# Kernel optimization log

Measured on AMD Instinct MI355X. Metric: run time of the kernel, lower is better.

## Reference

```python
import jax, jax.numpy as jnp
import numpy as np

N_NODES = 50000
N_EDGES = 800000
IN_DIM = 128
HID = 2 * IN_DIM          # GCNConv out channels = input_dims * 2
FC1 = 1024
FC2 = 512
N_ACT = 16
N_AGENTS = 8192
EPS = 1e-5


def setup_inputs() -> dict:
    key = jax.random.key(0)
    ks = jax.random.split(key, 12)
    def gl(k, shape):  # glorot-ish init for weights
        fan = shape[0]
        return jax.random.normal(k, shape, jnp.float32) / jnp.sqrt(jnp.float32(fan))
    return {
        "x": jax.random.normal(ks[0], (N_NODES, IN_DIM), jnp.float32),
        "edge_index": jax.random.randint(ks[1], (2, N_EDGES), 0, N_NODES, jnp.int32),
        "agent_idx": jax.random.randint(ks[2], (N_AGENTS,), 0, N_NODES, jnp.int32),
        "W_gcn": gl(ks[3], (IN_DIM, HID)),
        "b_gcn": jnp.zeros((HID,), jnp.float32),
        "W1": gl(ks[4], (HID, FC1)),
        "b1": jnp.zeros((FC1,), jnp.float32),
        "g1": jnp.ones((FC1,), jnp.float32),
        "be1": jnp.zeros((FC1,), jnp.float32),
        "W2": gl(ks[5], (FC1, FC2)),
        "b2": jnp.zeros((FC2,), jnp.float32),
        "g2": jnp.ones((FC2,), jnp.float32),
        "be2": jnp.zeros((FC2,), jnp.float32),
        "Wmu": gl(ks[6], (FC2, N_ACT)) * 0.003,
        "bmu": jnp.zeros((N_ACT,), jnp.float32),
    }


def _layernorm(h, g, b):
    mu = jnp.mean(h, axis=-1, keepdims=True)
    var = jnp.mean(jnp.square(h - mu), axis=-1, keepdims=True)
    return (h - mu) * jax.lax.rsqrt(var + EPS) * g + b


def _gcn_conv(x, edge_index, W, b):
    # PyG GCNConv: add self-loops, symmetric normalization, linear, scatter-add.
    n = x.shape[0]
    loop = jnp.arange(n, dtype=edge_index.dtype)
    src = jnp.concatenate([edge_index[0], loop])   # [E+N]
    dst = jnp.concatenate([edge_index[1], loop])   # [E+N]
    deg = jax.ops.segment_sum(jnp.ones_like(dst, jnp.float32), dst, num_segments=n)
    dis = jnp.where(deg > 0, jax.lax.rsqrt(jnp.maximum(deg, 1.0)), 0.0)
    norm = dis[src] * dis[dst]                     # [E+N]
    xw = x @ W                                     # [N, HID]
    msg = xw[src] * norm[:, None]                  # gather + scale
    return jax.ops.segment_sum(msg, dst, num_segments=n) + b


def reference(x, edge_index, agent_idx, W_gcn, b_gcn, W1, b1, g1, be1,
              W2, b2, g2, be2, Wmu, bmu):
    h = _gcn_conv(x, edge_index, W_gcn, b_gcn)     # [N, HID]
    h = h[agent_idx]                               # masked selection -> [A, HID]
    h = jax.nn.relu(h)
    h = jax.nn.relu(_layernorm(h @ W1 + b1, g1, be1))
    h = jax.nn.relu(_layernorm(h @ W2 + b2, g2, be2))
    return jax.nn.sigmoid(h @ Wmu + bmu)           # [A, N_ACT]
```

## Files before the change

kernel.cpp:

```cpp
#include <hip/hip_runtime.h>
#include <hip/hip_bf16.h>
#include <math.h>

#define N_NODES  50000
#define N_EDGES  800000
#define IN_DIM   128
#define HID      256
#define FC1      1024
#define FC2      512
#define N_ACT    16
#define N_AGENTS 8192

#define BK       64
#define LDK      72
#define BM       128
#define BN       128

#define EB_STRIDE    64

#define SCAT_CHUNK   2048
#define SCAT_BLOCKS  ((N_EDGES + SCAT_CHUNK - 1) / SCAT_CHUNK)
#define N_BUCKETS    196
#define BUCKET_CAP   4608
#define WTR_BLOCKS   208
#define CLAIM_BLOCKS (N_AGENTS / 256)

typedef short bf16x8 __attribute__((ext_vector_type(8)));
typedef float floatx4 __attribute__((ext_vector_type(4)));

__device__ __forceinline__ unsigned short f2b(float f) {
    union { float f; unsigned int i; } v;
    v.f = f;
    unsigned int lsb = (v.i >> 16) & 1u;
    v.i += 0x7fffu + lsb;
    return (unsigned short)(v.i >> 16);
}

__device__ __forceinline__ float b2f(unsigned short u) {
    union { unsigned int i; float f; } v;
    v.i = ((unsigned int)u) << 16;
    return v.f;
}

__device__ __forceinline__ void wtr_block(int b, int tid,
    const float* __restrict__ Wgcn, const float* __restrict__ W1,
    const float* __restrict__ W2, const float* __restrict__ Wmu,
    unsigned short* __restrict__ wgcn_t, unsigned short* __restrict__ w1_t,
    unsigned short* __restrict__ w2_t, unsigned short* __restrict__ wmu_t,
    unsigned short (*Ts)[72]) {
    const float* src; unsigned short* dstw; int K, N, tk, tn;
    if (b < 8)        { src = Wgcn; dstw = wgcn_t; K = IN_DIM; N = HID;  tk = b >> 2;        tn = b & 3; }
    else if (b < 72)  { int bb = b - 8;  src = W1; dstw = w1_t; K = HID;  N = FC1;  tk = bb >> 4; tn = bb & 15; }
    else if (b < 200) { int bb = b - 72; src = W2; dstw = w2_t; K = FC1;  N = FC2;  tk = bb >> 3; tn = bb & 7; }
    else              { int bb = b - 200; src = Wmu; dstw = wmu_t; K = FC2; N = N_ACT; tk = bb;   tn = 0; }
    int k0 = tk * 64, n0 = tn * 64;
    int r = tid >> 2;
    int cc = (tid & 3) * 16;
    if (n0 + cc < N) {
        const float* p = src + (size_t)(k0 + r) * N + n0 + cc;
        #pragma unroll
        for (int i = 0; i < 16; i += 4) {
            float4 v = *(const float4*)(p + i);
            Ts[r][cc + i + 0] = f2b(v.x);
            Ts[r][cc + i + 1] = f2b(v.y);
            Ts[r][cc + i + 2] = f2b(v.z);
            Ts[r][cc + i + 3] = f2b(v.w);
        }
    }
    __syncthreads();
    int n = tid >> 2;
    if (n0 + n < N) {
        bf16x8 o0, o1;
        #pragma unroll
        for (int i = 0; i < 8; ++i) o0[i] = (short)Ts[cc + i][n];
        #pragma unroll
        for (int i = 0; i < 8; ++i) o1[i] = (short)Ts[cc + 8 + i][n];
        unsigned short* q = dstw + (size_t)(n0 + n) * K + k0 + cc;
        *(bf16x8*)q = o0;
        *(bf16x8*)(q + 8) = o1;
    }
}

__global__ __launch_bounds__(256) void scat_k(const int* __restrict__ src,
                                              const int* __restrict__ dst,
                                              const int* __restrict__ agent_idx,
                                              int* __restrict__ nid,
                                              int* __restrict__ bcnt,
                                              unsigned long long* __restrict__ pairbuf,
                                              const float* __restrict__ Wgcn,
                                              const float* __restrict__ W1,
                                              const float* __restrict__ W2,
                                              const float* __restrict__ Wmu,
                                              unsigned short* __restrict__ wgcn_t,
                                              unsigned short* __restrict__ w1_t,
                                              unsigned short* __restrict__ w2_t,
                                              unsigned short* __restrict__ wmu_t) {
    __shared__ unsigned short Ts[64][72];
    __shared__ int hist[N_BUCKETS], base[N_BUCKETS], cur[N_BUCKETS];
    int tid = threadIdx.x;
    int blk = blockIdx.x;
    if (blk >= SCAT_BLOCKS) {
        int bb = blk - SCAT_BLOCKS;
        if (bb < WTR_BLOCKS) {
            wtr_block(bb, tid, Wgcn, W1, W2, Wmu, wgcn_t, w1_t, w2_t, wmu_t, Ts);
        } else {
            int i = (bb - WTR_BLOCKS) * 256 + tid;
            atomicCAS(&nid[agent_idx[i]], 0, i + 1);
        }
        return;
    }
    if (tid < N_BUCKETS) { hist[tid] = 0; cur[tid] = 0; }
    __syncthreads();
    int e0 = blk * SCAT_CHUNK;
    int dv[8];
    #pragma unroll
    for (int i = 0; i < 8; ++i) {
        int e = e0 + i * 256 + tid;
        dv[i] = (e < N_EDGES) ? dst[e] : -1;
        if (dv[i] >= 0) atomicAdd(&hist[dv[i] >> 8], 1);
    }
    __syncthreads();
    if (tid < N_BUCKETS && hist[tid] > 0)
        base[tid] = atomicAdd(&bcnt[tid], hist[tid]);
    __syncthreads();
    #pragma unroll
    for (int i = 0; i < 8; ++i) {
        int e = e0 + i * 256 + tid;
        if (e < N_EDGES) {
            int d = dv[i];
            int bk = d >> 8;
            int p = base[bk] + atomicAdd(&cur[bk], 1);
            if (p < BUCKET_CAP)
                pairbuf[(size_t)bk * BUCKET_CAP + p] =
                    ((unsigned long long)(unsigned)src[e] << 32) | (unsigned)d;
        }
    }
}

__global__ __launch_bounds__(256) void bucket_k(const int* __restrict__ bcnt,
                                                const unsigned long long* __restrict__ pairbuf,
                                                const int* __restrict__ nid,
                                                int* __restrict__ deg,
                                                int* __restrict__ ebuf) {
    __shared__ int nidl[256], lhist[256], lfill[256];
    int b = blockIdx.x, tid = threadIdx.x;
    int node = b * 256 + tid;
    nidl[tid] = (node < N_NODES) ? nid[node] : 0;
    lhist[tid] = 0;
    lfill[tid] = 0;
    __syncthreads();
    int n = bcnt[b];
    if (n > BUCKET_CAP) n = BUCKET_CAP;
    const unsigned long long* pb = pairbuf + (size_t)b * BUCKET_CAP;
    for (int i = tid; i < n; i += 256) {
        unsigned long long pr = pb[i];
        int d = (int)(unsigned)pr;
        int s = (int)(pr >> 32);
        int l = d & 255;
        atomicAdd(&lhist[l], 1);
        int cc = nidl[l];
        if (cc != 0) {
            int p = atomicAdd(&lfill[l], 1);
            if (p < EB_STRIDE) ebuf[((cc - 1) << 6) + p] = s;
        }
    }
    __syncthreads();
    if (node < N_NODES) deg[node] = lhist[tid];
}

__global__ __launch_bounds__(256) void accumx_k(const int* __restrict__ agent_idx,
                                                const int* __restrict__ nid,
                                                const int* __restrict__ deg,
                                                const int* __restrict__ ebuf,
                                                const float* __restrict__ x,
                                                unsigned short* __restrict__ agg) {
    int c = blockIdx.x * 4 + (threadIdx.x >> 6);
    int lane = threadIdx.x & 63;
    int n = agent_idx[c];
    float ax = 0.0f, ay = 0.0f;
    if (nid[n] == c + 1) {
        int dn_i = deg[n];
        int cnt = dn_i;
        if (cnt > EB_STRIDE) cnt = EB_STRIDE;
        float dn = rsqrtf((float)(dn_i + 1));
        const int* eb = ebuf + (c << 6);
        for (int i = 0; i < cnt; ++i) {
            int s = eb[i];
            float w = rsqrtf((float)(deg[s] + 1)) * dn;
            float2 u = *(const float2*)(x + (size_t)s * IN_DIM + lane * 2);
            ax += w * u.x;
            ay += w * u.y;
        }
        float2 u = *(const float2*)(x + (size_t)n * IN_DIM + lane * 2);
        float w2 = dn * dn;
        ax += w2 * u.x;
        ay += w2 * u.y;
    }
    unsigned int pk = (unsigned int)f2b(ax) | ((unsigned int)f2b(ay) << 16);
    *(unsigned int*)(agg + (size_t)c * IN_DIM + lane * 2) = pk;
}

__global__ __launch_bounds__(256) void gemm_gcn_k(const unsigned short* __restrict__ A,
                                                  const unsigned short* __restrict__ Bt,
                                                  const float* __restrict__ bias,
                                                  unsigned short* __restrict__ outb) {
    __shared__ unsigned short As[64][LDK];
    __shared__ unsigned short Bs[128][LDK];
    int bid = blockIdx.x;
    int tn = (bid >> 3) & 1;
    int tm = (bid & 7) + 8 * (bid >> 4);
    int tid = threadIdx.x;
    int lane = tid & 63, wave = tid >> 6;
    int r16 = lane & 15, quad = lane >> 4;
    int srow = tid >> 2, scol = (tid & 3) * 8;
    const int K = IN_DIM, N = HID;
    const unsigned short* pa0 = A + (size_t)(tm * 64 + srow) * K + scol;
    const unsigned short* pb0 = Bt + (size_t)(tn * 128 + srow) * K + scol;
    const unsigned short* pb1 = Bt + (size_t)(tn * 128 + srow + 64) * K + scol;

    floatx4 acc[4][2];
    #pragma unroll
    for (int i = 0; i < 4; ++i)
        #pragma unroll
        for (int j = 0; j < 2; ++j)
            acc[i][j] = (floatx4){0.0f, 0.0f, 0.0f, 0.0f};

    bf16x8 ra0[2], rb0[2], rb1[2];
    ra0[0] = *(const bf16x8*)pa0;        ra0[1] = *(const bf16x8*)(pa0 + 32);
    rb0[0] = *(const bf16x8*)pb0;        rb0[1] = *(const bf16x8*)(pb0 + 32);
    rb1[0] = *(const bf16x8*)pb1;        rb1[1] = *(const bf16x8*)(pb1 + 32);

    for (int k0 = 0; k0 < K; k0 += BK) {
        *(bf16x8*)&As[srow][scol]           = ra0[0];
        *(bf16x8*)&As[srow][scol + 32]      = ra0[1];
        *(bf16x8*)&Bs[srow][scol]           = rb0[0];
        *(bf16x8*)&Bs[srow][scol + 32]      = rb0[1];
        *(bf16x8*)&Bs[srow + 64][scol]      = rb1[0];
        *(bf16x8*)&Bs[srow + 64][scol + 32] = rb1[1];
        __syncthreads();
        if (k0 + BK < K) {
            ra0[0] = *(const bf16x8*)(pa0 + k0 + BK); ra0[1] = *(const bf16x8*)(pa0 + k0 + BK + 32);
            rb0[0] = *(const bf16x8*)(pb0 + k0 + BK); rb0[1] = *(const bf16x8*)(pb0 + k0 + BK + 32);
            rb1[0] = *(const bf16x8*)(pb1 + k0 + BK); rb1[1] = *(const bf16x8*)(pb1 + k0 + BK + 32);
        }
        #pragma unroll
        for (int h = 0; h < 2; ++h) {
            bf16x8 af[4], bfr[2];
            #pragma unroll
            for (int i = 0; i < 4; ++i)
                af[i] = *(const bf16x8*)&As[i * 16 + r16][h * 32 + quad * 8];
            #pragma unroll
            for (int j = 0; j < 2; ++j)
                bfr[j] = *(const bf16x8*)&Bs[wave * 32 + j * 16 + r16][h * 32 + quad * 8];
            #pragma unroll
            for (int i = 0; i < 4; ++i)
                #pragma unroll
                for (int j = 0; j < 2; ++j)
                    acc[i][j] = __builtin_amdgcn_mfma_f32_16x16x32_bf16(af[i], bfr[j], acc[i][j], 0, 0, 0);
        }
        __syncthreads();
    }

    #pragma unroll
    for (int j = 0; j < 2; ++j) {
        int ocol = tn * 128 + wave * 32 + j * 16 + r16;
        float bv = bias[ocol];
        #pragma unroll
        for (int i = 0; i < 4; ++i) {
            int orow = tm * 64 + i * 16 + quad * 4;
            #pragma unroll
            for (int r = 0; r < 4; ++r) {
                float v = acc[i][j][r] + bv;
                if (v < 0.0f) v = 0.0f;
                outb[(size_t)(orow + r) * N + ocol] = f2b(v);
            }
        }
    }
}

__global__ __launch_bounds__(256) void gemm_fc1_k(const unsigned short* __restrict__ h_node,
                                                  const int* __restrict__ agent,
                                                  const int* __restrict__ nid,
                                                  const unsigned short* __restrict__ Bt,
                                                  const float* __restrict__ bias,
                                                  unsigned short* __restrict__ outb) {
    __shared__ unsigned short As[BM][LDK];
    __shared__ unsigned short Bs[BN][LDK];
    int bid = blockIdx.x;
    int tn = (bid >> 3) & 7;
    int tm = (bid & 7) + 8 * (bid >> 6);
    int tid = threadIdx.x;
    int lane = tid & 63, wave = tid >> 6;
    int wm = wave >> 1, wn = wave & 1;
    int r16 = lane & 15, quad = lane >> 4;
    int srow = tid >> 2, scol = (tid & 3) * 8;
    const int K = HID, N = FC1;
    int c0 = nid[agent[tm * BM + srow]] - 1;
    int c1 = nid[agent[tm * BM + srow + 64]] - 1;
    const unsigned short* pa0 = h_node + (size_t)c0 * K + scol;
    const unsigned short* pa1 = h_node + (size_t)c1 * K + scol;
    const unsigned short* pb0 = Bt + (size_t)(tn * BN + srow) * K + scol;
    const unsigned short* pb1 = Bt + (size_t)(tn * BN + srow + 64) * K + scol;

    floatx4 acc[4][4];
    #pragma unroll
    for (int i = 0; i < 4; ++i)
        #pragma unroll
        for (int j = 0; j < 4; ++j)
            acc[i][j] = (floatx4){0.0f, 0.0f, 0.0f, 0.0f};

    bf16x8 ra0[2], ra1[2], rb0[2], rb1[2];
    ra0[0] = *(const bf16x8*)pa0;        ra0[1] = *(const bf16x8*)(pa0 + 32);
    ra1[0] = *(const bf16x8*)pa1;        ra1[1] = *(const bf16x8*)(pa1 + 32);
    rb0[0] = *(const bf16x8*)pb0;        rb0[1] = *(const bf16x8*)(pb0 + 32);
    rb1[0] = *(const bf16x8*)pb1;        rb1[1] = *(const bf16x8*)(pb1 + 32);

    for (int k0 = 0; k0 < K; k0 += BK) {
        *(bf16x8*)&As[srow][scol]           = ra0[0];
        *(bf16x8*)&As[srow][scol + 32]      = ra0[1];
        *(bf16x8*)&As[srow + 64][scol]      = ra1[0];
        *(bf16x8*)&As[srow + 64][scol + 32] = ra1[1];
        *(bf16x8*)&Bs[srow][scol]           = rb0[0];
        *(bf16x8*)&Bs[srow][scol + 32]      = rb0[1];
        *(bf16x8*)&Bs[srow + 64][scol]      = rb1[0];
        *(bf16x8*)&Bs[srow + 64][scol + 32] = rb1[1];
        __syncthreads();
        if (k0 + BK < K) {
            ra0[0] = *(const bf16x8*)(pa0 + k0 + BK); ra0[1] = *(const bf16x8*)(pa0 + k0 + BK + 32);
            ra1[0] = *(const bf16x8*)(pa1 + k0 + BK); ra1[1] = *(const bf16x8*)(pa1 + k0 + BK + 32);
            rb0[0] = *(const bf16x8*)(pb0 + k0 + BK); rb0[1] = *(const bf16x8*)(pb0 + k0 + BK + 32);
            rb1[0] = *(const bf16x8*)(pb1 + k0 + BK); rb1[1] = *(const bf16x8*)(pb1 + k0 + BK + 32);
        }
        #pragma unroll
        for (int h = 0; h < 2; ++h) {
            bf16x8 af[4], bfr[4];
            #pragma unroll
            for (int i = 0; i < 4; ++i)
                af[i] = *(const bf16x8*)&As[wm * 64 + i * 16 + r16][h * 32 + quad * 8];
            #pragma unroll
            for (int j = 0; j < 4; ++j)
                bfr[j] = *(const bf16x8*)&Bs[wn * 64 + j * 16 + r16][h * 32 + quad * 8];
            #pragma unroll
            for (int i = 0; i < 4; ++i)
                #pragma unroll
                for (int j = 0; j < 4; ++j)
                    acc[i][j] = __builtin_amdgcn_mfma_f32_16x16x32_bf16(af[i], bfr[j], acc[i][j], 0, 0, 0);
        }
        __syncthreads();
    }

    float bvj[4];
    #pragma unroll
    for (int j = 0; j < 4; ++j) bvj[j] = bias[tn * BN + wn * 64 + j * 16 + r16];

    #pragma unroll
    for (int i = 0; i < 4; ++i) {
        #pragma unroll
        for (int r = 0; r < 4; ++r) {
            int orow = tm * BM + wm * 64 + i * 16 + quad * 4 + r;
            #pragma unroll
            for (int j = 0; j < 4; ++j) {
                int ocol = tn * BN + wn * 64 + j * 16 + r16;
                outb[(size_t)orow * N + ocol] = f2b(acc[i][j][r] + bvj[j]);
            }
        }
    }
}

__global__ __launch_bounds__(256) void ln1_k(const unsigned short* __restrict__ zb,
                                             const float* __restrict__ g1,
                                             const float* __restrict__ be1,
                                             unsigned short* __restrict__ zbn) {
    int row = blockIdx.x * 4 + (threadIdx.x >> 6);
    int lane = threadIdx.x & 63;
    const unsigned short* p = zb + (size_t)row * FC1 + lane * 16;
    bf16x8 a0 = *(const bf16x8*)p;
    bf16x8 a1 = *(const bf16x8*)(p + 8);
    float v[16];
    #pragma unroll
    for (int i = 0; i < 8; ++i) {
        v[i]     = b2f((unsigned short)a0[i]);
        v[8 + i] = b2f((unsigned short)a1[i]);
    }
    float s = 0.0f, s2 = 0.0f;
    #pragma unroll
    for (int i = 0; i < 16; ++i) { s += v[i]; s2 += v[i] * v[i]; }
    #pragma unroll
    for (int m = 1; m < 64; m <<= 1) {
        s  += __shfl_xor(s, m);
        s2 += __shfl_xor(s2, m);
    }
    float mean = s * (1.0f / FC1);
    float var = s2 * (1.0f / FC1) - mean * mean;
    float inv = rsqrtf(var + 1e-5f);
    const float4* g4 = (const float4*)(g1 + lane * 16);
    const float4* b4 = (const float4*)(be1 + lane * 16);
    float gg[16], bb[16];
    #pragma unroll
    for (int q = 0; q < 4; ++q) {
        float4 gv = g4[q], bv = b4[q];
        gg[q * 4 + 0] = gv.x; gg[q * 4 + 1] = gv.y; gg[q * 4 + 2] = gv.z; gg[q * 4 + 3] = gv.w;
        bb[q * 4 + 0] = bv.x; bb[q * 4 + 1] = bv.y; bb[q * 4 + 2] = bv.z; bb[q * 4 + 3] = bv.w;
    }
    bf16x8 o0, o1;
    #pragma unroll
    for (int i = 0; i < 8; ++i) {
        float w = (v[i] - mean) * inv * gg[i] + bb[i];
        if (w < 0.0f) w = 0.0f;
        o0[i] = (short)f2b(w);
    }
    #pragma unroll
    for (int i = 0; i < 8; ++i) {
        float w = (v[8 + i] - mean) * inv * gg[8 + i] + bb[8 + i];
        if (w < 0.0f) w = 0.0f;
        o1[i] = (short)f2b(w);
    }
    unsigned short* q = zbn + (size_t)row * FC1 + lane * 16;
    *(bf16x8*)q = o0;
    *(bf16x8*)(q + 8) = o1;
}

__global__ __launch_bounds__(256) void gemm_fc2_k(const unsigned short* __restrict__ A,
                                                  const unsigned short* __restrict__ Bt,
                                                  const float* __restrict__ bias,
                                                  unsigned short* __restrict__ outb) {
    __shared__ unsigned short As[64][LDK];
    __shared__ unsigned short Bs[128][LDK];
    int bid = blockIdx.x;
    int tn = (bid >> 3) & 3;
    int tm = (bid & 7) + 8 * (bid >> 5);
    int tid = threadIdx.x;
    int lane = tid & 63, wave = tid >> 6;
    int r16 = lane & 15, quad = lane >> 4;
    int srow = tid >> 2, scol = (tid & 3) * 8;
    const int K = FC1, N = FC2;
    const unsigned short* pa0 = A + (size_t)(tm * 64 + srow) * K + scol;
    const unsigned short* pb0 = Bt + (size_t)(tn * 128 + srow) * K + scol;
    const unsigned short* pb1 = Bt + (size_t)(tn * 128 + srow + 64) * K + scol;

    floatx4 acc[4][2];
    #pragma unroll
    for (int i = 0; i < 4; ++i)
        #pragma unroll
        for (int j = 0; j < 2; ++j)
            acc[i][j] = (floatx4){0.0f, 0.0f, 0.0f, 0.0f};

    bf16x8 ra0[2], rb0[2], rb1[2];
    ra0[0] = *(const bf16x8*)pa0;        ra0[1] = *(const bf16x8*)(pa0 + 32);
    rb0[0] = *(const bf16x8*)pb0;        rb0[1] = *(const bf16x8*)(pb0 + 32);
    rb1[0] = *(const bf16x8*)pb1;        rb1[1] = *(const bf16x8*)(pb1 + 32);

    for (int k0 = 0; k0 < K; k0 += BK) {
        *(bf16x8*)&As[srow][scol]           = ra0[0];
        *(bf16x8*)&As[srow][scol + 32]      = ra0[1];
        *(bf16x8*)&Bs[srow][scol]           = rb0[0];
        *(bf16x8*)&Bs[srow][scol + 32]      = rb0[1];
        *(bf16x8*)&Bs[srow + 64][scol]      = rb1[0];
        *(bf16x8*)&Bs[srow + 64][scol + 32] = rb1[1];
        __syncthreads();
        if (k0 + BK < K) {
            ra0[0] = *(const bf16x8*)(pa0 + k0 + BK); ra0[1] = *(const bf16x8*)(pa0 + k0 + BK + 32);
            rb0[0] = *(const bf16x8*)(pb0 + k0 + BK); rb0[1] = *(const bf16x8*)(pb0 + k0 + BK + 32);
            rb1[0] = *(const bf16x8*)(pb1 + k0 + BK); rb1[1] = *(const bf16x8*)(pb1 + k0 + BK + 32);
        }
        #pragma unroll
        for (int h = 0; h < 2; ++h) {
            bf16x8 af[4], bfr[2];
            #pragma unroll
            for (int i = 0; i < 4; ++i)
                af[i] = *(const bf16x8*)&As[i * 16 + r16][h * 32 + quad * 8];
            #pragma unroll
            for (int j = 0; j < 2; ++j)
                bfr[j] = *(const bf16x8*)&Bs[wave * 32 + j * 16 + r16][h * 32 + quad * 8];
            #pragma unroll
            for (int i = 0; i < 4; ++i)
                #pragma unroll
                for (int j = 0; j < 2; ++j)
                    acc[i][j] = __builtin_amdgcn_mfma_f32_16x16x32_bf16(af[i], bfr[j], acc[i][j], 0, 0, 0);
        }
        __syncthreads();
    }

    #pragma unroll
    for (int j = 0; j < 2; ++j) {
        int ocol = tn * 128 + wave * 32 + j * 16 + r16;
        float bv = bias[ocol];
        #pragma unroll
        for (int i = 0; i < 4; ++i) {
            int orow = tm * 64 + i * 16 + quad * 4;
            #pragma unroll
            for (int r = 0; r < 4; ++r)
                outb[(size_t)(orow + r) * N + ocol] = f2b(acc[i][j][r] + bv);
        }
    }
}

__global__ __launch_bounds__(256) void ln2head_k(const unsigned short* __restrict__ z,
                                                 const float* __restrict__ g2,
                                                 const float* __restrict__ be2,
                                                 const unsigned short* __restrict__ wmu_t,
                                                 const float* __restrict__ bmu,
                                                 float* __restrict__ out) {
    __shared__ unsigned short Hs[16][520];
    __shared__ float hred[4][64][4];
    int tid = threadIdx.x;
    int tm = blockIdx.x;
    {
        int row = tid >> 4;
        int sub = tid & 15;
        const unsigned short* src = z + (size_t)(tm * 16 + row) * FC2 + sub * 32;
        bf16x8 a0 = *(const bf16x8*)(src);
        bf16x8 a1 = *(const bf16x8*)(src + 8);
        bf16x8 a2 = *(const bf16x8*)(src + 16);
        bf16x8 a3 = *(const bf16x8*)(src + 24);
        float v[32];
        #pragma unroll
        for (int i = 0; i < 8; ++i) {
            v[i]      = b2f((unsigned short)a0[i]);
            v[8 + i]  = b2f((unsigned short)a1[i]);
            v[16 + i] = b2f((unsigned short)a2[i]);
            v[24 + i] = b2f((unsigned short)a3[i]);
        }
        float s = 0.0f, s2 = 0.0f;
        #pragma unroll
        for (int i = 0; i < 32; ++i) { s += v[i]; s2 += v[i] * v[i]; }
        #pragma unroll
        for (int m = 1; m < 16; m <<= 1) {
            s  += __shfl_xor(s, m);
            s2 += __shfl_xor(s2, m);
        }
        float mean = s * (1.0f / FC2);
        float var = s2 * (1.0f / FC2) - mean * mean;
        float inv = rsqrtf(var + 1e-5f);
        #pragma unroll
        for (int i = 0; i < 32; ++i) {
            int c = sub * 32 + i;
            float w = (v[i] - mean) * inv * g2[c] + be2[c];
            if (w < 0.0f) w = 0.0f;
            Hs[row][c] = f2b(w);
        }
    }
    __syncthreads();
    int lane = tid & 63, wave = tid >> 6;
    int r16 = lane & 15, quad = lane >> 4;
    floatx4 acc = {0.0f, 0.0f, 0.0f, 0.0f};
    #pragma unroll
    for (int st = 0; st < 4; ++st) {
        bf16x8 a = *(const bf16x8*)&Hs[r16][wave * 128 + st * 32 + quad * 8];
        bf16x8 b = *(const bf16x8*)(wmu_t + (size_t)r16 * FC2 + wave * 128 + st * 32 + quad * 8);
        acc = __builtin_amdgcn_mfma_f32_16x16x32_bf16(a, b, acc, 0, 0, 0);
    }
    #pragma unroll
    for (int r = 0; r < 4; ++r) hred[wave][lane][r] = acc[r];
    __syncthreads();
    if (wave == 0) {
        #pragma unroll
        for (int r = 0; r < 4; ++r) {
            float v = hred[0][lane][r] + hred[1][lane][r] + hred[2][lane][r] + hred[3][lane][r];
            v += bmu[r16];
            v = 1.0f / (1.0f + expf(-v));
            out[(size_t)(tm * 16 + quad * 4 + r) * N_ACT + r16] = v;
        }
    }
}

extern "C" void kernel_launch(void* const* d_in, const int* in_sizes, int n_in,
                              void* d_out, int out_size, void* d_ws, size_t ws_size,
                              hipStream_t stream) {
    const float* x    = (const float*)d_in[0];
    const int*   ei   = (const int*)d_in[1];
    const int*   agent= (const int*)d_in[2];
    const float* Wgcn = (const float*)d_in[3];
    const float* bgcn = (const float*)d_in[4];
    const float* W1   = (const float*)d_in[5];
    const float* b1   = (const float*)d_in[6];
    const float* g1   = (const float*)d_in[7];
    const float* be1  = (const float*)d_in[8];
    const float* W2   = (const float*)d_in[9];
    const float* b2   = (const float*)d_in[10];
    const float* g2   = (const float*)d_in[11];
    const float* be2  = (const float*)d_in[12];
    const float* Wmu  = (const float*)d_in[13];
    const float* bmu  = (const float*)d_in[14];
    float* out = (float*)d_out;

    const int* srcp = ei;
    const int* dstp = ei + N_EDGES;

    char* ws = (char*)d_ws;
    size_t off = 0;
    char* zero_base = ws;
    int* nid  = (int*)(ws + off);      off += ((size_t)N_NODES * 4 + 255) & ~(size_t)255;
    int* bcnt = (int*)(ws + off);      off += ((size_t)N_BUCKETS * 4 + 255) & ~(size_t)255;
    size_t zero_bytes = off;
    int* deg  = (int*)(ws + off);      off += ((size_t)N_NODES * 4 + 255) & ~(size_t)255;
    unsigned long long* pairbuf = (unsigned long long*)(ws + off);
    off += ((size_t)N_BUCKETS * BUCKET_CAP * 8 + 255) & ~(size_t)255;
    int* ebuf = (int*)(ws + off);      off += ((size_t)N_AGENTS * EB_STRIDE * 4 + 255) & ~(size_t)255;
    unsigned short* wgcn_t = (unsigned short*)(ws + off); off += ((size_t)IN_DIM * HID * 2 + 255) & ~(size_t)255;
    unsigned short* w1_t   = (unsigned short*)(ws + off); off += ((size_t)HID * FC1 * 2 + 255) & ~(size_t)255;
    unsigned short* w2_t   = (unsigned short*)(ws + off); off += ((size_t)FC1 * FC2 * 2 + 255) & ~(size_t)255;
    unsigned short* wmu_t  = (unsigned short*)(ws + off); off += ((size_t)FC2 * N_ACT * 2 + 255) & ~(size_t)255;
    unsigned short* agg    = (unsigned short*)(ws + off); off += ((size_t)N_AGENTS * IN_DIM * 2 + 255) & ~(size_t)255;
    unsigned short* h_node = (unsigned short*)(ws + off); off += ((size_t)N_AGENTS * HID * 2 + 255) & ~(size_t)255;
    unsigned short* zb  = (unsigned short*)(ws + off);    off += ((size_t)N_AGENTS * FC1 * 2 + 255) & ~(size_t)255;
    unsigned short* zbn = (unsigned short*)(ws + off);    off += ((size_t)N_AGENTS * FC1 * 2 + 255) & ~(size_t)255;
    unsigned short* zb2 = (unsigned short*)(ws + off);    off += ((size_t)N_AGENTS * FC2 * 2 + 255) & ~(size_t)255;

    hipMemsetAsync(zero_base, 0, zero_bytes, stream);

    scat_k<<<SCAT_BLOCKS + WTR_BLOCKS + CLAIM_BLOCKS, 256, 0, stream>>>(
        srcp, dstp, agent, nid, bcnt, pairbuf,
        Wgcn, W1, W2, Wmu, wgcn_t, w1_t, w2_t, wmu_t);

    bucket_k<<<N_BUCKETS, 256, 0, stream>>>(bcnt, pairbuf, nid, deg, ebuf);

    accumx_k<<<N_AGENTS / 4, 256, 0, stream>>>(agent, nid, deg, ebuf, x, agg);

    gemm_gcn_k<<<(HID / 128) * (N_AGENTS / 64), 256, 0, stream>>>(agg, wgcn_t, bgcn, h_node);

    gemm_fc1_k<<<(FC1 / BN) * (N_AGENTS / BM), 256, 0, stream>>>(h_node, agent, nid, w1_t, b1, zb);

    ln1_k<<<N_AGENTS / 4, 256, 0, stream>>>(zb, g1, be1, zbn);

    gemm_fc2_k<<<(FC2 / 128) * (N_AGENTS / 64), 256, 0, stream>>>(zbn, w2_t, b2, zb2);

    ln2head_k<<<N_AGENTS / 16, 256, 0, stream>>>(zb2, g2, be2, wmu_t, bmu, out);
}
```

Before: 188.5 us.

## Load GEMM tiles directly into LDS with XOR swizzle, enlarge fc2 tile

The three GEMM kernels now stage A and B tiles with global_load_lds, which writes straight from global memory into XOR-swizzled shared memory. This replaces the register-staged copy and the padded LDK layout. The fc2 GEMM moves from 64x128 to 128x128 tiles with a 2x2 wave layout, halving its grid. The GCN accumulation kernel loads each edge's source index and norm weight once per lane and broadcasts them with shuffles instead of re-reading them serially. In exchange, the register prefetch of the next tile is dropped, so global loads no longer overlap with MFMA work within a block.

```diff
diff --git a/kernel.cpp b/kernel.cpp
--- a/kernel.cpp
+++ b/kernel.cpp
@@ -12,7 +12,6 @@
 #define N_AGENTS 8192
 
 #define BK       64
-#define LDK      72
 #define BM       128
 #define BN       128
 
@@ -40,6 +39,12 @@
     union { unsigned int i; float f; } v;
     v.i = ((unsigned int)u) << 16;
     return v.f;
+}
+
+__device__ __forceinline__ void gl_lds(const unsigned short* g, unsigned short* l) {
+    __builtin_amdgcn_global_load_lds(
+        (const __attribute__((address_space(1))) void*)g,
+        (__attribute__((address_space(3))) void*)l, 16, 0, 0);
 }
 
 __device__ __forceinline__ void wtr_block(int b, int tid,
@@ -180,13 +185,14 @@
     float ax = 0.0f, ay = 0.0f;
     if (nid[n] == c + 1) {
         int dn_i = deg[n];
-        int cnt = dn_i;
-        if (cnt > EB_STRIDE) cnt = EB_STRIDE;
+        int cnt = dn_i < EB_STRIDE ? dn_i : EB_STRIDE;
         float dn = rsqrtf((float)(dn_i + 1));
         const int* eb = ebuf + (c << 6);
+        int ej = (lane < cnt) ? eb[lane] : n;
+        float wl = rsqrtf((float)(deg[ej] + 1)) * dn;
         for (int i = 0; i < cnt; ++i) {
-            int s = eb[i];
-            float w = rsqrtf((float)(deg[s] + 1)) * dn;
+            int s = __shfl(ej, i);
+            float w = __shfl(wl, i);
             float2 u = *(const float2*)(x + (size_t)s * IN_DIM + lane * 2);
             ax += w * u.x;
             ay += w * u.y;
@@ -200,23 +206,22 @@
     *(unsigned int*)(agg + (size_t)c * IN_DIM + lane * 2) = pk;
 }
 
+
 __global__ __launch_bounds__(256) void gemm_gcn_k(const unsigned short* __restrict__ A,
                                                   const unsigned short* __restrict__ Bt,
                                                   const float* __restrict__ bias,
                                                   unsigned short* __restrict__ outb) {
-    __shared__ unsigned short As[64][LDK];
-    __shared__ unsigned short Bs[128][LDK];
+    __shared__ unsigned short As[64][64];
+    __shared__ unsigned short Bs[128][64];
     int bid = blockIdx.x;
     int tn = (bid >> 3) & 1;
     int tm = (bid & 7) + 8 * (bid >> 4);
     int tid = threadIdx.x;
     int lane = tid & 63, wave = tid >> 6;
     int r16 = lane & 15, quad = lane >> 4;
-    int srow = tid >> 2, scol = (tid & 3) * 8;
+    int lr = (tid >> 3) & 7;
+    int swz = ((tid & 7) ^ lr) * 8;
     const int K = IN_DIM, N = HID;
-    const unsigned short* pa0 = A + (size_t)(tm * 64 + srow) * K + scol;
-    const unsigned short* pb0 = Bt + (size_t)(tn * 128 + srow) * K + scol;
-    const unsigned short* pb1 = Bt + (size_t)(tn * 128 + srow + 64) * K + scol;
 
     floatx4 acc[4][2];
     #pragma unroll
@@ -225,40 +230,33 @@
         for (int j = 0; j < 2; ++j)
             acc[i][j] = (floatx4){0.0f, 0.0f, 0.0f, 0.0f};
 
-    bf16x8 ra0[2], rb0[2], rb1[2];
-    ra0[0] = *(const bf16x8*)pa0;        ra0[1] = *(const bf16x8*)(pa0 + 32);
-    rb0[0] = *(const bf16x8*)pb0;        rb0[1] = *(const bf16x8*)(pb0 + 32);
-    rb1[0] = *(const bf16x8*)pb1;        rb1[1] = *(const bf16x8*)(pb1 + 32);
-
     for (int k0 = 0; k0 < K; k0 += BK) {
-        *(bf16x8*)&As[srow][scol]           = ra0[0];
-        *(bf16x8*)&As[srow][scol + 32]      = ra0[1];
-        *(bf16x8*)&Bs[srow][scol]           = rb0[0];
-        *(bf16x8*)&Bs[srow][scol + 32]      = rb0[1];
-        *(bf16x8*)&Bs[srow + 64][scol]      = rb1[0];
-        *(bf16x8*)&Bs[srow + 64][scol + 32] = rb1[1];
+        if (k0) __syncthreads();
+        #pragma unroll
+        for (int q = 0; q < 2; ++q)
+            gl_lds(A + (size_t)(tm * 64 + (wave * 2 + q) * 8 + lr) * K + k0 + swz,
+                   &As[(wave * 2 + q) * 8][0]);
+        #pragma unroll
+        for (int q = 0; q < 4; ++q)
+            gl_lds(Bt + (size_t)(tn * 128 + (wave * 4 + q) * 8 + lr) * K + k0 + swz,
+                   &Bs[(wave * 4 + q) * 8][0]);
         __syncthreads();
-        if (k0 + BK < K) {
-            ra0[0] = *(const bf16x8*)(pa0 + k0 + BK); ra0[1] = *(const bf16x8*)(pa0 + k0 + BK + 32);
-            rb0[0] = *(const bf16x8*)(pb0 + k0 + BK); rb0[1] = *(const bf16x8*)(pb0 + k0 + BK + 32);
-            rb1[0] = *(const bf16x8*)(pb1 + k0 + BK); rb1[1] = *(const bf16x8*)(pb1 + k0 + BK + 32);
-        }
         #pragma unroll
         for (int h = 0; h < 2; ++h) {
+            int col = (h * 32 + quad * 8) ^ ((r16 & 7) << 3);
             bf16x8 af[4], bfr[2];
             #pragma unroll
             for (int i = 0; i < 4; ++i)
-                af[i] = *(const bf16x8*)&As[i * 16 + r16][h * 32 + quad * 8];
+                af[i] = *(const bf16x8*)&As[i * 16 + r16][col];
             #pragma unroll
             for (int j = 0; j < 2; ++j)
-                bfr[j] = *(const bf16x8*)&Bs[wave * 32 + j * 16 + r16][h * 32 + quad * 8];
+                bfr[j] = *(const bf16x8*)&Bs[wave * 32 + j * 16 + r16][col];
             #pragma unroll
             for (int i = 0; i < 4; ++i)
                 #pragma unroll
                 for (int j = 0; j < 2; ++j)
                     acc[i][j] = __builtin_amdgcn_mfma_f32_16x16x32_bf16(af[i], bfr[j], acc[i][j], 0, 0, 0);
         }
-        __syncthreads();
     }
 
     #pragma unroll
@@ -284,8 +282,8 @@
                                                   const unsigned short* __restrict__ Bt,
                                                   const float* __restrict__ bias,
                                                   unsigned short* __restrict__ outb) {
-    __shared__ unsigned short As[BM][LDK];
-    __shared__ unsigned short Bs[BN][LDK];
+    __shared__ unsigned short As[BM][64];
+    __shared__ unsigned short Bs[BN][64];
     int bid = blockIdx.x;
     int tn = (bid >> 3) & 7;
     int tm = (bid & 7) + 8 * (bid >> 6);
@@ -293,14 +291,14 @@
     int lane = tid & 63, wave = tid >> 6;
     int wm = wave >> 1, wn = wave & 1;
     int r16 = lane & 15, quad = lane >> 4;
-    int srow = tid >> 2, scol = (tid & 3) * 8;
+    int lr = (tid >> 3) & 7;
+    int swz = ((tid & 7) ^ lr) * 8;
     const int K = HID, N = FC1;
-    int c0 = nid[agent[tm * BM + srow]] - 1;
-    int c1 = nid[agent[tm * BM + srow + 64]] - 1;
-    const unsigned short* pa0 = h_node + (size_t)c0 * K + scol;
-    const unsigned short* pa1 = h_node + (size_t)c1 * K + scol;
-    const unsigned short* pb0 = Bt + (size_t)(tn * BN + srow) * K + scol;
-    const unsigned short* pb1 = Bt + (size_t)(tn * BN + srow + 64) * K + scol;
+
+    int cA[4];
+    #pragma unroll
+    for (int q = 0; q < 4; ++q)
+        cA[q] = nid[agent[tm * BM + (wave * 4 + q) * 8 + lr]] - 1;
 
     floatx4 acc[4][4];
     #pragma unroll
@@ -309,44 +307,32 @@
         for (int j = 0; j < 4; ++j)
             acc[i][j] = (floatx4){0.0f, 0.0f, 0.0f, 0.0f};
 
-    bf16x8 ra0[2], ra1[2], rb0[2], rb1[2];
-    ra0[0] = *(const bf16x8*)pa0;        ra0[1] = *(const bf16x8*)(pa0 + 32);
-    ra1[0] = *(const bf16x8*)pa1;        ra1[1] = *(const bf16x8*)(pa1 + 32);
-    rb0[0] = *(const bf16x8*)pb0;        rb0[1] = *(const bf16x8*)(pb0 + 32);
-    rb1[0] = *(const bf16x8*)pb1;        rb1[1] = *(const bf16x8*)(pb1 + 32);
-
     for (int k0 = 0; k0 < K; k0 += BK) {
-        *(bf16x8*)&As[srow][scol]           = ra0[0];
-        *(bf16x8*)&As[srow][scol + 32]      = ra0[1];
-        *(bf16x8*)&As[srow + 64][scol]      = ra1[0];
-        *(bf16x8*)&As[srow + 64][scol + 32] = ra1[1];
-        *(bf16x8*)&Bs[srow][scol]           = rb0[0];
-        *(bf16x8*)&Bs[srow][scol + 32]      = rb0[1];
-        *(bf16x8*)&Bs[srow + 64][scol]      = rb1[0];
-        *(bf16x8*)&Bs[srow + 64][scol + 32] = rb1[1];
+        if (k0) __syncthreads();
+        #pragma unroll
+        for (int q = 0; q < 4; ++q) {
+            gl_lds(h_node + (size_t)cA[q] * K + k0 + swz,
+                   &As[(wave * 4 + q) * 8][0]);
+            gl_lds(Bt + (size_t)(tn * BN + (wave * 4 + q) * 8 + lr) * K + k0 + swz,
+                   &Bs[(wave * 4 + q) * 8][0]);
+        }
         __syncthreads();
-        if (k0 + BK < K) {
-            ra0[0] = *(const bf16x8*)(pa0 + k0 + BK); ra0[1] = *(const bf16x8*)(pa0 + k0 + BK + 32);
-            ra1[0] = *(const bf16x8*)(pa1 + k0 + BK); ra1[1] = *(const bf16x8*)(pa1 + k0 + BK + 32);
-            rb0[0] = *(const bf16x8*)(pb0 + k0 + BK); rb0[1] = *(const bf16x8*)(pb0 + k0 + BK + 32);
-            rb1[0] = *(const bf16x8*)(pb1 + k0 + BK); rb1[1] = *(const bf16x8*)(pb1 + k0 + BK + 32);
-        }
         #pragma unroll
         for (int h = 0; h < 2; ++h) {
+            int col = (h * 32 + quad * 8) ^ ((r16 & 7) << 3);
             bf16x8 af[4], bfr[4];
             #pragma unroll
             for (int i = 0; i < 4; ++i)
-                af[i] = *(const bf16x8*)&As[wm * 64 + i * 16 + r16][h * 32 + quad * 8];
+                af[i] = *(const bf16x8*)&As[wm * 64 + i * 16 + r16][col];
             #pragma unroll
             for (int j = 0; j < 4; ++j)
-                bfr[j] = *(const bf16x8*)&Bs[wn * 64 + j * 16 + r16][h * 32 + quad * 8];
+                bfr[j] = *(const bf16x8*)&Bs[wn * 64 + j * 16 + r16][col];
             #pragma unroll
             for (int i = 0; i < 4; ++i)
                 #pragma unroll
                 for (int j = 0; j < 4; ++j)
                     acc[i][j] = __builtin_amdgcn_mfma_f32_16x16x32_bf16(af[i], bfr[j], acc[i][j], 0, 0, 0);
         }
-        __syncthreads();
     }
 
     float bvj[4];
@@ -424,73 +410,68 @@
                                                   const unsigned short* __restrict__ Bt,
                                                   const float* __restrict__ bias,
                                                   unsigned short* __restrict__ outb) {
-    __shared__ unsigned short As[64][LDK];
-    __shared__ unsigned short Bs[128][LDK];
+    __shared__ unsigned short As[BM][64];
+    __shared__ unsigned short Bs[BN][64];
     int bid = blockIdx.x;
     int tn = (bid >> 3) & 3;
     int tm = (bid & 7) + 8 * (bid >> 5);
     int tid = threadIdx.x;
     int lane = tid & 63, wave = tid >> 6;
+    int wm = wave >> 1, wn = wave & 1;
     int r16 = lane & 15, quad = lane >> 4;
-    int srow = tid >> 2, scol = (tid & 3) * 8;
+    int lr = (tid >> 3) & 7;
+    int swz = ((tid & 7) ^ lr) * 8;
     const int K = FC1, N = FC2;
-    const unsigned short* pa0 = A + (size_t)(tm * 64 + srow) * K + scol;
-    const unsigned short* pb0 = Bt + (size_t)(tn * 128 + srow) * K + scol;
-    const unsigned short* pb1 = Bt + (size_t)(tn * 128 + srow + 64) * K + scol;
-
-    floatx4 acc[4][2];
+
+    floatx4 acc[4][4];
     #pragma unroll
     for (int i = 0; i < 4; ++i)
         #pragma unroll
-        for (int j = 0; j < 2; ++j)
+        for (int j = 0; j < 4; ++j)
             acc[i][j] = (floatx4){0.0f, 0.0f, 0.0f, 0.0f};
 
-    bf16x8 ra0[2], rb0[2], rb1[2];
-    ra0[0] = *(const bf16x8*)pa0;        ra0[1] = *(const bf16x8*)(pa0 + 32);
-    rb0[0] = *(const bf16x8*)pb0;        rb0[1] = *(const bf16x8*)(pb0 + 32);
-    rb1[0] = *(const bf16x8*)pb1;        rb1[1] = *(const bf16x8*)(pb1 + 32);
-
     for (int k0 = 0; k0 < K; k0 += BK) {
-        *(bf16x8*)&As[srow][scol]           = ra0[0];
-        *(bf16x8*)&As[srow][scol + 32]      = ra0[1];
-        *(bf16x8*)&Bs[srow][scol]           = rb0[0];
-        *(bf16x8*)&Bs[srow][scol + 32]      = rb0[1];
-        *(bf16x8*)&Bs[srow + 64][scol]      = rb1[0];
-        *(bf16x8*)&Bs[srow + 64][scol + 32] = rb1[1];
+        if (k0) __syncthreads();
+        #pragma unroll
+        for (int q = 0; q < 4; ++q) {
+            gl_lds(A + (size_t)(tm * BM + (wave * 4 + q) * 8 + lr) * K + k0 + swz,
+                   &As[(wave * 4 + q) * 8][0]);
+            gl_lds(Bt + (size_t)(tn * BN + (wave * 4 + q) * 8 + lr) * K + k0 + swz,
+                   &Bs[(wave * 4 + q) * 8][0]);
+        }
         __syncthreads();
-        if (k0 + BK < K) {
-            ra0[0] = *(const bf16x8*)(pa0 + k0 + BK); ra0[1] = *(const bf16x8*)(pa0 + k0 + BK + 32);
-            rb0[0] = *(const bf16x8*)(pb0 + k0 + BK); rb0[1] = *(const bf16x8*)(pb0 + k0 + BK + 32);
-            rb1[0] = *(const bf16x8*)(pb1 + k0 + BK); rb1[1] = *(const bf16x8*)(pb1 + k0 + BK + 32);
-        }
         #pragma unroll
         for (int h = 0; h < 2; ++h) {
-            bf16x8 af[4], bfr[2];
+            int col = (h * 32 + quad * 8) ^ ((r16 & 7) << 3);
+            bf16x8 af[4], bfr[4];
             #pragma unroll
             for (int i = 0; i < 4; ++i)
-                af[i] = *(const bf16x8*)&As[i * 16 + r16][h * 32 + quad * 8];
-            #pragma unroll
-            for (int j = 0; j < 2; ++j)
-                bfr[j] = *(const bf16x8*)&Bs[wave * 32 + j * 16 + r16][h * 32 + quad * 8];
+                af[i] = *(const bf16x8*)&As[wm * 64 + i * 16 + r16][col];
+            #pragma unroll
+            for (int j = 0; j < 4; ++j)
+                bfr[j] = *(const bf16x8*)&Bs[wn * 64 + j * 16 + r16][col];
             #pragma unroll
             for (int i = 0; i < 4; ++i)
                 #pragma unroll
-                for (int j = 0; j < 2; ++j)
+                for (int j = 0; j < 4; ++j)
                     acc[i][j] = __builtin_amdgcn_mfma_f32_16x16x32_bf16(af[i], bfr[j], acc[i][j], 0, 0, 0);
         }
-        __syncthreads();
-    }
-
-    #pragma unroll
-    for (int j = 0; j < 2; ++j) {
-        int ocol = tn * 128 + wave * 32 + j * 16 + r16;
-        float bv = bias[ocol];
-        #pragma unroll
-        for (int i = 0; i < 4; ++i) {
-            int orow = tm * 64 + i * 16 + quad * 4;
-            #pragma unroll
-            for (int r = 0; r < 4; ++r)
-                outb[(size_t)(orow + r) * N + ocol] = f2b(acc[i][j][r] + bv);
+    }
+
+    float bvj[4];
+    #pragma unroll
+    for (int j = 0; j < 4; ++j) bvj[j] = bias[tn * BN + wn * 64 + j * 16 + r16];
+
+    #pragma unroll
+    for (int i = 0; i < 4; ++i) {
+        #pragma unroll
+        for (int r = 0; r < 4; ++r) {
+            int orow = tm * BM + wm * 64 + i * 16 + quad * 4 + r;
+            #pragma unroll
+            for (int j = 0; j < 4; ++j) {
+                int ocol = tn * BN + wn * 64 + j * 16 + r16;
+                outb[(size_t)orow * N + ocol] = f2b(acc[i][j][r] + bvj[j]);
+            }
         }
     }
 }
@@ -623,7 +604,7 @@
 
     ln1_k<<<N_AGENTS / 4, 256, 0, stream>>>(zb, g1, be1, zbn);
 
-    gemm_fc2_k<<<(FC2 / 128) * (N_AGENTS / 64), 256, 0, stream>>>(zbn, w2_t, b2, zb2);
+    gemm_fc2_k<<<(FC2 / 128) * (N_AGENTS / 128), 256, 0, stream>>>(zbn, w2_t, b2, zb2);
 
     ln2head_k<<<N_AGENTS / 16, 256, 0, stream>>>(zb2, g2, be2, wmu_t, bmu, out);
 }
```

Result: faster. 182.4 us (-3.3%).
